# Kernel optimization log

Hardware: AMD Instinct MI355X
Metric: run time of the kernel (lower is better)

The kernel has to match this reference:

```python
import jax, jax.numpy as jnp
import numpy as np

B, N, D, H = 8, 2048, 256, 8
HD = D // H  # head_dim = 32
LN_EPS = 1e-5


def setup_inputs() -> dict:
    key = jax.random.key(0)
    ks = jax.random.split(key, 8)
    x = jax.random.normal(ks[0], (B, N, D), dtype=jnp.float32)
    # dense 0/1 adjacency with guaranteed self-loops (avoids all -inf softmax rows)
    adj = jax.random.randint(ks[1], (B, N, N), 0, 2, dtype=jnp.int32)
    adj = jnp.maximum(adj, jnp.eye(N, dtype=jnp.int32)[None, :, :])
    s = 0.02
    Wq = jax.random.normal(ks[2], (D, D), dtype=jnp.float32) * s
    Wk = jax.random.normal(ks[3], (D, D), dtype=jnp.float32) * s
    Wv = jax.random.normal(ks[4], (D, D), dtype=jnp.float32) * s
    Wo = jax.random.normal(ks[5], (D, D), dtype=jnp.float32) * s
    zeros = jnp.zeros((D,), dtype=jnp.float32)
    return {
        "x": x, "adjacency": adj,
        "Wq": Wq, "bq": zeros, "Wk": Wk, "bk": zeros,
        "Wv": Wv, "bv": zeros, "Wo": Wo, "bo": zeros,
        "gamma": jnp.ones((D,), dtype=jnp.float32), "beta": zeros,
    }


def reference(x, adjacency, Wq, bq, Wk, bk, Wv, bv, Wo, bo, gamma, beta):
    b, n, d = x.shape
    q = (x @ Wq + bq).reshape(b, n, H, HD)
    k = (x @ Wk + bk).reshape(b, n, H, HD)
    v = (x @ Wv + bv).reshape(b, n, H, HD)
    # scores: [B, N(query), M(key), H]
    scores = jnp.einsum('bnhd,bmhd->bnmh', q, k) / jnp.sqrt(jnp.float32(HD))
    mask = (adjacency == 0)[..., None]  # [B,N,M,1] broadcasts over heads
    scores = jnp.where(mask, -jnp.inf, scores)
    weights = jax.nn.softmax(scores, axis=2)  # softmax over key axis m
    # dropout is identity in eval mode
    attended = jnp.einsum('bnmh,bmhd->bnhd', weights, v).reshape(b, n, d)
    out = attended @ Wo + bo
    out = out + x  # residual (output.shape == x.shape since input_dim == output_dim)
    mu = jnp.mean(out, axis=-1, keepdims=True)
    var = jnp.mean(jnp.square(out - mu), axis=-1, keepdims=True)
    return (out - mu) * jax.lax.rsqrt(var + LN_EPS) * gamma + beta
```

## Files before the change

### kernel.cpp

```cpp
#include <hip/hip_runtime.h>
#include <hip/hip_bf16.h>
#include <cstdint>
#include <cstddef>

#define B_ 8
#define N_ 2048
#define D_ 256
#define H_ 8
#define HD_ 32
#define LN_EPS 1e-5f
#define QSCALE 0.25506275f

typedef __attribute__((ext_vector_type(8))) short short8;
typedef __attribute__((ext_vector_type(4))) float f32x4;
typedef __attribute__((ext_vector_type(16))) float f32x16;

static __device__ __forceinline__ float exp2v(float x) {
#if __has_builtin(__builtin_amdgcn_exp2f)
    return __builtin_amdgcn_exp2f(x);
#else
    float r;
    asm("v_exp_f32 %0, %1" : "=v"(r) : "v"(x));
    return r;
#endif
}

static __device__ __forceinline__ unsigned short f2bf(float f) {
    union { float f; unsigned int u; } v; v.f = f;
    unsigned int r = v.u + 0x7fffu + ((v.u >> 16) & 1u);
    return (unsigned short)(r >> 16);
}

static __device__ __forceinline__ unsigned int cvtpk(float lo, float hi) {
    unsigned int d;
    asm("v_cvt_pk_bf16_f32 %0, %1, %2" : "=v"(d) : "v"(lo), "v"(hi));
    return d;
}

__global__ __launch_bounds__(256) void k_prep_w(const float* __restrict__ w0, const float* __restrict__ w1,
                                                const float* __restrict__ w2, const float* __restrict__ w3,
                                                unsigned short* __restrict__ wt) {
    int c = blockIdx.x, mat = blockIdx.y, k = threadIdx.x;
    const float* w = (mat == 0) ? w0 : (mat == 1) ? w1 : (mat == 2) ? w2 : w3;
    wt[((size_t)(mat * 256 + c)) * 256 + k] = f2bf(w[k * 256 + c]);
}

__global__ __launch_bounds__(256) void k_maskF(const int* __restrict__ adj,
                                               unsigned int* __restrict__ mbgT2) {
    __shared__ unsigned int bits[64][66];
    int tid = threadIdx.x, lane = tid & 63, wv = tid >> 6;
    int b = blockIdx.x >> 5, rg = blockIdx.x & 31;

    const int* base = adj + ((size_t)(b * N_ + rg * 64 + wv * 16)) * N_ + lane;
#pragma unroll 1
    for (int i = 0; i < 16; ++i) {
        const int* prow = base + (size_t)i * N_;
#pragma unroll
        for (int half = 0; half < 2; ++half) {
            int v[16];
#pragma unroll
            for (int j = 0; j < 16; ++j)
                v[j] = prow[half * 1024 + j * 64];
            __builtin_amdgcn_sched_barrier(0);
#pragma unroll
            for (int j = 0; j < 16; ++j) {
                unsigned long long m = __ballot(v[j] != 0);
                if (lane == 0)
                    *reinterpret_cast<unsigned long long*>(&bits[wv * 16 + i][half * 32 + 2 * j]) = m;
            }
        }
    }
    __syncthreads();

    int h = lane >> 5, l31 = lane & 31;
    const unsigned int M[5] = {0x0000FFFFu, 0x00FF00FFu, 0x0F0F0F0Fu, 0x33333333u, 0x55555555u};
#pragma unroll
    for (int j = 0; j < 16; ++j) {
        int kw = wv * 16 + j;
        unsigned int w = bits[lane][kw];
#pragma unroll
        for (int si = 0; si < 5; ++si) {
            int s = 16 >> si;
            unsigned int m = M[si];
            unsigned int t = (unsigned int)__shfl_xor((int)w, s, 64);
            unsigned int a = (w & m) | ((t & m) << s);
            unsigned int c = (w & ~m) | ((t >> s) & m);
            w = (lane & s) ? c : a;
        }
        int k = kw * 32 + l31;
        int kp = (k & ~7) | ((k & 3) << 1) | ((k >> 2) & 1);
        mbgT2[((size_t)(b * 64 + rg * 2 + h)) * 2048 + kp] = w;
    }
}

__global__ __launch_bounds__(256) void k_qkv(const float* __restrict__ x,
                                             const unsigned short* __restrict__ wt,
                                             const float* __restrict__ bq, const float* __restrict__ bk,
                                             const float* __restrict__ bv,
                                             unsigned short* __restrict__ Qb, unsigned short* __restrict__ Kb,
                                             unsigned short* __restrict__ Vs) {
    int mat = blockIdx.y;
    int lane = threadIdx.x & 63;
    int wv = threadIdx.x >> 6;
    int row0 = blockIdx.x * 64 + wv * 16;
    int l15 = lane & 15, lg = lane >> 4;
    const float* bias = (mat == 0) ? bq : (mat == 1) ? bk : bv;
    const float qs = (mat == 0) ? QSCALE : 1.0f;
    const unsigned short* wm = wt + (size_t)mat * 65536;

    short8 af[8];
    const float* xrow = x + (size_t)(row0 + l15) * 256 + lg * 8;
#pragma unroll
    for (int kk = 0; kk < 8; ++kk) {
        float4 a = *reinterpret_cast<const float4*>(xrow + kk * 32);
        float4 b = *reinterpret_cast<const float4*>(xrow + kk * 32 + 4);
        union { short8 s8; unsigned int u[4]; } t;
        t.u[0] = cvtpk(a.x, a.y); t.u[1] = cvtpk(a.z, a.w);
        t.u[2] = cvtpk(b.x, b.y); t.u[3] = cvtpk(b.z, b.w);
        af[kk] = t.s8;
    }

    int b = row0 >> 11;
    int nbase = (row0 & 2047) + lg * 4;

    for (int ci = 0; ci < 16; ++ci) {
        const unsigned short* wrow = wm + (size_t)(ci * 16 + l15) * 256 + lg * 8;
        f32x4 acc = {0.f, 0.f, 0.f, 0.f};
#pragma unroll
        for (int kk = 0; kk < 8; ++kk) {
            short8 bfg = *reinterpret_cast<const short8*>(wrow + kk * 32);
            acc = __builtin_amdgcn_mfma_f32_16x16x32_bf16(af[kk], bfg, acc, 0, 0, 0);
        }
        int col = ci * 16 + l15;
        float bcol = bias[col];
        int h = col >> 5, hd = col & 31;
        if (mat < 2) {
            unsigned short* dst = (mat == 0) ? Qb : Kb;
#pragma unroll
            for (int r = 0; r < 4; ++r) {
                size_t off = ((size_t)(b * 8 + h) * 2048 + nbase + r) * 32 + hd;
                dst[off] = f2bf((acc[r] + bcol) * qs);
            }
        } else {
            size_t off = (size_t)(b * 8 + h) * 65536
                       + ((size_t)(nbase >> 4) * 32 + hd) * 16 + (nbase & 15);
            ushort4 o;
            o.x = f2bf(acc[0] + bcol); o.y = f2bf(acc[1] + bcol);
            o.z = f2bf(acc[2] + bcol); o.w = f2bf(acc[3] + bcol);
            *reinterpret_cast<ushort4*>(Vs + off) = o;
        }
    }
}

#define SL(j, offs) asm("s_load_dwordx2 %0, %1, " offs : "=s"(m##j) : "s"(mbase))
#define SLOAD16() do { \
    SL(0, "0x0");  SL(1, "0x8");  SL(2, "0x10"); SL(3, "0x18"); \
    SL(4, "0x20"); SL(5, "0x28"); SL(6, "0x30"); SL(7, "0x38"); \
    SL(8, "0x40"); SL(9, "0x48"); SL(10, "0x50"); SL(11, "0x58"); \
    SL(12, "0x60"); SL(13, "0x68"); SL(14, "0x70"); SL(15, "0x78"); } while (0)
#define CND(d, s_, mj) asm("v_cndmask_b32 %0, 0, %1, %2" : "=v"(d) : "v"(s_), "s"(mj))

__global__ __launch_bounds__(256, 5) void k_attn(const unsigned short* __restrict__ Qb,
                                                 const unsigned short* __restrict__ Kb,
                                                 const unsigned short* __restrict__ Vs,
                                                 const unsigned int* __restrict__ mbgT2,
                                                 unsigned short* __restrict__ att) {
    int tid = threadIdx.x;
    int lane = tid & 63;
    int l31 = lane & 31, hi = lane >> 5;
    int b = blockIdx.x & 7;
    int hg = (blockIdx.x >> 3) & 1;
    int qt32 = blockIdx.x >> 4;
    int q0 = qt32 * 32;
    int head = hg * 4 + (tid >> 6);
    int bh = b * 8 + head;

    const unsigned short* Qh = Qb + (size_t)bh * N_ * HD_;
    const unsigned short* Kh = Kb + (size_t)bh * N_ * HD_;
    const unsigned short* Vh = Vs + (size_t)bh * 65536;

    short8 qf0 = *reinterpret_cast<const short8*>(Qh + (size_t)(q0 + l31) * HD_ + hi * 8);
    short8 qf1 = *reinterpret_cast<const short8*>(Qh + (size_t)(q0 + l31) * HD_ + hi * 8 + 16);
    const unsigned short* krow = Kh + (size_t)l31 * HD_ + hi * 8;
    const unsigned short* vfp = Vh + (size_t)l31 * 16 + hi * 8;

    unsigned long long mbase = (unsigned long long)(mbgT2 + (size_t)(b * 64 + qt32) * 2048);
    unsigned long long m0, m1, m2, m3, m4, m5, m6, m7, m8, m9, m10, m11, m12, m13, m14, m15;
    SLOAD16();

    const f32x16 fz = {0.f,0.f,0.f,0.f,0.f,0.f,0.f,0.f,0.f,0.f,0.f,0.f,0.f,0.f,0.f,0.f};
    f32x16 attacc = fz;
    float lsum = 0.f;

#pragma unroll 2
    for (int t = 0; t < 64; ++t) {
        short8 kf0 = *reinterpret_cast<const short8*>(krow + (size_t)t * 1024);
        short8 kf1 = *reinterpret_cast<const short8*>(krow + (size_t)t * 1024 + 16);
        short8 vf0 = *reinterpret_cast<const short8*>(vfp + (size_t)t * 1024);
        short8 vf1 = *reinterpret_cast<const short8*>(vfp + (size_t)t * 1024 + 512);

        f32x16 s = __builtin_amdgcn_mfma_f32_32x32x16_bf16(kf0, qf0, fz, 0, 0, 0);
        s = __builtin_amdgcn_mfma_f32_32x32x16_bf16(kf1, qf1, s, 0, 0, 0);

        float e0 = exp2v(s[0]),  e1 = exp2v(s[1]),  e2 = exp2v(s[2]),  e3 = exp2v(s[3]);
        float e4 = exp2v(s[4]),  e5 = exp2v(s[5]),  e6 = exp2v(s[6]),  e7 = exp2v(s[7]);
        float e8 = exp2v(s[8]),  e9 = exp2v(s[9]),  e10 = exp2v(s[10]), e11 = exp2v(s[11]);
        float e12 = exp2v(s[12]), e13 = exp2v(s[13]), e14 = exp2v(s[14]), e15 = exp2v(s[15]);

        asm volatile("s_waitcnt lgkmcnt(0)"
                     : "+s"(m0), "+s"(m1), "+s"(m2), "+s"(m3), "+s"(m4), "+s"(m5), "+s"(m6), "+s"(m7),
                       "+s"(m8), "+s"(m9), "+s"(m10), "+s"(m11), "+s"(m12), "+s"(m13), "+s"(m14), "+s"(m15));

        float p0, p1, p2, p3, p4, p5, p6, p7, p8, p9, p10, p11, p12, p13, p14, p15;
        CND(p0, e0, m0);   CND(p1, e1, m1);   CND(p2, e2, m2);   CND(p3, e3, m3);
        CND(p4, e4, m4);   CND(p5, e5, m5);   CND(p6, e6, m6);   CND(p7, e7, m7);
        CND(p8, e8, m8);   CND(p9, e9, m9);   CND(p10, e10, m10); CND(p11, e11, m11);
        CND(p12, e12, m12); CND(p13, e13, m13); CND(p14, e14, m14); CND(p15, e15, m15);

        lsum += ((p0 + p1) + (p2 + p3)) + ((p4 + p5) + (p6 + p7))
              + ((p8 + p9) + (p10 + p11)) + ((p12 + p13) + (p14 + p15));

        unsigned int pd[4][2];
        pd[0][0] = cvtpk(p0, p1);   pd[0][1] = cvtpk(p2, p3);
        pd[1][0] = cvtpk(p4, p5);   pd[1][1] = cvtpk(p6, p7);
        pd[2][0] = cvtpk(p8, p9);   pd[2][1] = cvtpk(p10, p11);
        pd[3][0] = cvtpk(p12, p13); pd[3][1] = cvtpk(p14, p15);

        mbase += 128;
        SLOAD16();

        asm("v_permlane32_swap_b32 %0, %1" : "+v"(pd[0][0]), "+v"(pd[1][0]));
        asm("v_permlane32_swap_b32 %0, %1" : "+v"(pd[0][1]), "+v"(pd[1][1]));
        asm("v_permlane32_swap_b32 %0, %1" : "+v"(pd[2][0]), "+v"(pd[3][0]));
        asm("v_permlane32_swap_b32 %0, %1" : "+v"(pd[2][1]), "+v"(pd[3][1]));

        union { short8 s8; unsigned int u[4]; } bf0, bf1;
        bf0.u[0] = pd[0][0]; bf0.u[1] = pd[0][1]; bf0.u[2] = pd[1][0]; bf0.u[3] = pd[1][1];
        bf1.u[0] = pd[2][0]; bf1.u[1] = pd[2][1]; bf1.u[2] = pd[3][0]; bf1.u[3] = pd[3][1];

        attacc = __builtin_amdgcn_mfma_f32_32x32x16_bf16(vf0, bf0.s8, attacc, 0, 0, 0);
        attacc = __builtin_amdgcn_mfma_f32_32x32x16_bf16(vf1, bf1.s8, attacc, 0, 0, 0);
    }

    lsum += __shfl_xor(lsum, 32, 64);
    float rcp = 1.f / lsum;

    unsigned short* arow = att + ((size_t)b * N_ + q0 + l31) * D_ + head * HD_;
#pragma unroll
    for (int g = 0; g < 4; ++g) {
        ushort4 o;
        o.x = f2bf(attacc[4 * g + 0] * rcp);
        o.y = f2bf(attacc[4 * g + 1] * rcp);
        o.z = f2bf(attacc[4 * g + 2] * rcp);
        o.w = f2bf(attacc[4 * g + 3] * rcp);
        *reinterpret_cast<ushort4*>(arow + 8 * g + 4 * hi) = o;
    }
}

__global__ __launch_bounds__(256) void k_outln(const unsigned short* __restrict__ att,
                                               const unsigned short* __restrict__ wot,
                                               const float* __restrict__ bo,
                                               const float* __restrict__ x,
                                               const float* __restrict__ gamma, const float* __restrict__ beta,
                                               float* __restrict__ out) {
    int lane = threadIdx.x & 63, wv = threadIdx.x >> 6;
    int l15 = lane & 15, lg = lane >> 4;
    int row0 = blockIdx.x * 64 + wv * 16;

    short8 af[8];
    const unsigned short* arow = att + (size_t)(row0 + l15) * 256 + lg * 8;
#pragma unroll
    for (int kk = 0; kk < 8; ++kk)
        af[kk] = *reinterpret_cast<const short8*>(arow + kk * 32);

    float v[16][4];
#pragma unroll
    for (int ci = 0; ci < 16; ++ci) {
        const unsigned short* wrow = wot + (size_t)(ci * 16 + l15) * 256 + lg * 8;
        f32x4 acc = {0.f, 0.f, 0.f, 0.f};
#pragma unroll
        for (int kk = 0; kk < 8; ++kk) {
            short8 bfg = *reinterpret_cast<const short8*>(wrow + kk * 32);
            acc = __builtin_amdgcn_mfma_f32_16x16x32_bf16(af[kk], bfg, acc, 0, 0, 0);
        }
        float bcol = bo[ci * 16 + l15];
#pragma unroll
        for (int r = 0; r < 4; ++r)
            v[ci][r] = acc[r] + bcol + x[(size_t)(row0 + lg * 4 + r) * 256 + ci * 16 + l15];
    }

    float sum[4] = {0.f, 0.f, 0.f, 0.f}, sq[4] = {0.f, 0.f, 0.f, 0.f};
#pragma unroll
    for (int ci = 0; ci < 16; ++ci)
#pragma unroll
        for (int r = 0; r < 4; ++r) {
            sum[r] += v[ci][r];
            sq[r] += v[ci][r] * v[ci][r];
        }
#pragma unroll
    for (int d = 1; d < 16; d <<= 1)
#pragma unroll
        for (int r = 0; r < 4; ++r) {
            sum[r] += __shfl_xor(sum[r], d, 64);
            sq[r] += __shfl_xor(sq[r], d, 64);
        }

    float mu[4], rs[4];
#pragma unroll
    for (int r = 0; r < 4; ++r) {
        mu[r] = sum[r] * (1.f / 256.f);
        float var = sq[r] * (1.f / 256.f) - mu[r] * mu[r];
        rs[r] = rsqrtf(var + LN_EPS);
    }

#pragma unroll
    for (int ci = 0; ci < 16; ++ci) {
        float g = gamma[ci * 16 + l15], be = beta[ci * 16 + l15];
#pragma unroll
        for (int r = 0; r < 4; ++r)
            out[(size_t)(row0 + lg * 4 + r) * 256 + ci * 16 + l15] = (v[ci][r] - mu[r]) * rs[r] * g + be;
    }
}

extern "C" void kernel_launch(void* const* d_in, const int* in_sizes, int n_in,
                              void* d_out, int out_size, void* d_ws, size_t ws_size,
                              hipStream_t stream) {
    (void)in_sizes; (void)n_in; (void)out_size; (void)ws_size;
    const float* x     = (const float*)d_in[0];
    const int*   adj   = (const int*)d_in[1];
    const float* Wq    = (const float*)d_in[2];
    const float* bq    = (const float*)d_in[3];
    const float* Wk    = (const float*)d_in[4];
    const float* bk    = (const float*)d_in[5];
    const float* Wv    = (const float*)d_in[6];
    const float* bv    = (const float*)d_in[7];
    const float* Wo    = (const float*)d_in[8];
    const float* bo    = (const float*)d_in[9];
    const float* gamma = (const float*)d_in[10];
    const float* beta  = (const float*)d_in[11];
    float* out = (float*)d_out;

    char* ws = (char*)d_ws;
    unsigned short* wt   = (unsigned short*)ws; ws += (size_t)4 * 256 * 256 * 2;
    unsigned short* Qb   = (unsigned short*)ws; ws += (size_t)B_ * H_ * N_ * HD_ * 2;
    unsigned short* Kb   = (unsigned short*)ws; ws += (size_t)B_ * H_ * N_ * HD_ * 2;
    unsigned short* Vs   = (unsigned short*)ws; ws += (size_t)B_ * H_ * N_ * HD_ * 2;
    unsigned short* att  = (unsigned short*)ws; ws += (size_t)16384 * 256 * 2;
    unsigned int*   mbgT2 = (unsigned int*)ws;  ws += (size_t)B_ * 64 * 2048 * 4 + 8192;

    k_prep_w<<<dim3(256, 4), 256, 0, stream>>>(Wq, Wk, Wv, Wo, wt);
    k_maskF<<<256, 256, 0, stream>>>(adj, mbgT2);
    k_qkv<<<dim3(256, 3), 256, 0, stream>>>(x, wt, bq, bk, bv, Qb, Kb, Vs);
    k_attn<<<1024, 256, 0, stream>>>(Qb, Kb, Vs, mbgT2, att);
    k_outln<<<256, 256, 0, stream>>>(att, wt + 3 * 65536, bo, x, gamma, beta, out);
}
```

Baseline: 187.8 us.

## Store Q/K/V in fragment-swizzled layout, vectorize stores, widen mask kernel

Q and K are now written by k_qkv in the same 32-row tiled, fragment-ordered layout as V, using swapped MFMA operands so each lane emits a contiguous ushort4 store. This lets k_attn fetch Q/K fragments with lane-linear contiguous loads instead of strided row loads. The output LayerNorm kernel also swaps MFMA operands so each lane owns one row, giving float4 loads and stores of x, gamma, beta and out and a shorter cross-lane reduction. The mask kernel doubles its threads per block to 512, so each wave handles half as many rows. The layout change must stay consistent across producer and consumer or attention results will be wrong.

```diff
diff --git a/kernel.cpp b/kernel.cpp
--- a/kernel.cpp
+++ b/kernel.cpp
@@ -45,15 +45,15 @@
     wt[((size_t)(mat * 256 + c)) * 256 + k] = f2bf(w[k * 256 + c]);
 }
 
-__global__ __launch_bounds__(256) void k_maskF(const int* __restrict__ adj,
+__global__ __launch_bounds__(512) void k_maskF(const int* __restrict__ adj,
                                                unsigned int* __restrict__ mbgT2) {
     __shared__ unsigned int bits[64][66];
     int tid = threadIdx.x, lane = tid & 63, wv = tid >> 6;
     int b = blockIdx.x >> 5, rg = blockIdx.x & 31;
 
-    const int* base = adj + ((size_t)(b * N_ + rg * 64 + wv * 16)) * N_ + lane;
+    const int* base = adj + ((size_t)(b * N_ + rg * 64 + wv * 8)) * N_ + lane;
 #pragma unroll 1
-    for (int i = 0; i < 16; ++i) {
+    for (int i = 0; i < 8; ++i) {
         const int* prow = base + (size_t)i * N_;
 #pragma unroll
         for (int half = 0; half < 2; ++half) {
@@ -66,7 +66,7 @@
             for (int j = 0; j < 16; ++j) {
                 unsigned long long m = __ballot(v[j] != 0);
                 if (lane == 0)
-                    *reinterpret_cast<unsigned long long*>(&bits[wv * 16 + i][half * 32 + 2 * j]) = m;
+                    *reinterpret_cast<unsigned long long*>(&bits[wv * 8 + i][half * 32 + 2 * j]) = m;
             }
         }
     }
@@ -75,8 +75,8 @@
     int h = lane >> 5, l31 = lane & 31;
     const unsigned int M[5] = {0x0000FFFFu, 0x00FF00FFu, 0x0F0F0F0Fu, 0x33333333u, 0x55555555u};
 #pragma unroll
-    for (int j = 0; j < 16; ++j) {
-        int kw = wv * 16 + j;
+    for (int j = 0; j < 8; ++j) {
+        int kw = wv * 8 + j;
         unsigned int w = bits[lane][kw];
 #pragma unroll
         for (int si = 0; si < 5; ++si) {
@@ -97,7 +97,7 @@
                                              const unsigned short* __restrict__ wt,
                                              const float* __restrict__ bq, const float* __restrict__ bk,
                                              const float* __restrict__ bv,
-                                             unsigned short* __restrict__ Qb, unsigned short* __restrict__ Kb,
+                                             unsigned short* __restrict__ Qts, unsigned short* __restrict__ Ks,
                                              unsigned short* __restrict__ Vs) {
     int mat = blockIdx.y;
     int lane = threadIdx.x & 63;
@@ -123,27 +123,44 @@
     int b = row0 >> 11;
     int nbase = (row0 & 2047) + lg * 4;
 
-    for (int ci = 0; ci < 16; ++ci) {
-        const unsigned short* wrow = wm + (size_t)(ci * 16 + l15) * 256 + lg * 8;
-        f32x4 acc = {0.f, 0.f, 0.f, 0.f};
-#pragma unroll
-        for (int kk = 0; kk < 8; ++kk) {
-            short8 bfg = *reinterpret_cast<const short8*>(wrow + kk * 32);
-            acc = __builtin_amdgcn_mfma_f32_16x16x32_bf16(af[kk], bfg, acc, 0, 0, 0);
-        }
-        int col = ci * 16 + l15;
-        float bcol = bias[col];
-        int h = col >> 5, hd = col & 31;
-        if (mat < 2) {
-            unsigned short* dst = (mat == 0) ? Qb : Kb;
-#pragma unroll
-            for (int r = 0; r < 4; ++r) {
-                size_t off = ((size_t)(b * 8 + h) * 2048 + nbase + r) * 32 + hd;
-                dst[off] = f2bf((acc[r] + bcol) * qs);
+    if (mat < 2) {
+        unsigned short* dst = (mat == 0) ? Qts : Ks;
+        int n = (row0 & 2047) + l15;
+        for (int ci = 0; ci < 16; ++ci) {
+            const unsigned short* wrow = wm + (size_t)(ci * 16 + l15) * 256 + lg * 8;
+            f32x4 acc = {0.f, 0.f, 0.f, 0.f};
+#pragma unroll
+            for (int kk = 0; kk < 8; ++kk) {
+                short8 bfg = *reinterpret_cast<const short8*>(wrow + kk * 32);
+                acc = __builtin_amdgcn_mfma_f32_16x16x32_bf16(bfg, af[kk], acc, 0, 0, 0);
             }
-        } else {
-            size_t off = (size_t)(b * 8 + h) * 65536
-                       + ((size_t)(nbase >> 4) * 32 + hd) * 16 + (nbase & 15);
+            int col0 = ci * 16 + lg * 4;
+            float4 b4 = *reinterpret_cast<const float4*>(bias + col0);
+            int h = col0 >> 5;
+            int hd0 = col0 & 31;
+            size_t off = (size_t)(b * 8 + h) * 65536 + (size_t)(n >> 5) * 1024
+                       + (size_t)(hd0 >> 4) * 512
+                       + (size_t)((((hd0 >> 3) & 1) * 32 + (n & 31))) * 8 + (hd0 & 7);
+            ushort4 o;
+            o.x = f2bf((acc[0] + b4.x) * qs); o.y = f2bf((acc[1] + b4.y) * qs);
+            o.z = f2bf((acc[2] + b4.z) * qs); o.w = f2bf((acc[3] + b4.w) * qs);
+            *reinterpret_cast<ushort4*>(dst + off) = o;
+        }
+    } else {
+        for (int ci = 0; ci < 16; ++ci) {
+            const unsigned short* wrow = wm + (size_t)(ci * 16 + l15) * 256 + lg * 8;
+            f32x4 acc = {0.f, 0.f, 0.f, 0.f};
+#pragma unroll
+            for (int kk = 0; kk < 8; ++kk) {
+                short8 bfg = *reinterpret_cast<const short8*>(wrow + kk * 32);
+                acc = __builtin_amdgcn_mfma_f32_16x16x32_bf16(af[kk], bfg, acc, 0, 0, 0);
+            }
+            int col = ci * 16 + l15;
+            float bcol = bias[col];
+            int h = col >> 5, hd = col & 31;
+            int posb = nbase & 31;
+            size_t off = (size_t)(b * 8 + h) * 65536 + (size_t)(nbase >> 5) * 1024
+                       + (posb >> 4) * 512 + ((((posb >> 3) & 1) * 32 + hd)) * 8 + (posb & 7);
             ushort4 o;
             o.x = f2bf(acc[0] + bcol); o.y = f2bf(acc[1] + bcol);
             o.z = f2bf(acc[2] + bcol); o.w = f2bf(acc[3] + bcol);
@@ -160,7 +177,7 @@
     SL(12, "0x60"); SL(13, "0x68"); SL(14, "0x70"); SL(15, "0x78"); } while (0)
 #define CND(d, s_, mj) asm("v_cndmask_b32 %0, 0, %1, %2" : "=v"(d) : "v"(s_), "s"(mj))
 
-__global__ __launch_bounds__(256, 5) void k_attn(const unsigned short* __restrict__ Qb,
+__global__ __launch_bounds__(256, 5) void k_attn(const unsigned short* __restrict__ Qts,
                                                  const unsigned short* __restrict__ Kb,
                                                  const unsigned short* __restrict__ Vs,
                                                  const unsigned int* __restrict__ mbgT2,
@@ -175,14 +192,14 @@
     int head = hg * 4 + (tid >> 6);
     int bh = b * 8 + head;
 
-    const unsigned short* Qh = Qb + (size_t)bh * N_ * HD_;
-    const unsigned short* Kh = Kb + (size_t)bh * N_ * HD_;
+    const unsigned short* Qh = Qts + (size_t)bh * 65536 + (size_t)qt32 * 1024 + (size_t)lane * 8;
+    const unsigned short* Kh = Kb + (size_t)bh * 65536;
     const unsigned short* Vh = Vs + (size_t)bh * 65536;
 
-    short8 qf0 = *reinterpret_cast<const short8*>(Qh + (size_t)(q0 + l31) * HD_ + hi * 8);
-    short8 qf1 = *reinterpret_cast<const short8*>(Qh + (size_t)(q0 + l31) * HD_ + hi * 8 + 16);
-    const unsigned short* krow = Kh + (size_t)l31 * HD_ + hi * 8;
-    const unsigned short* vfp = Vh + (size_t)l31 * 16 + hi * 8;
+    short8 qf0 = *reinterpret_cast<const short8*>(Qh);
+    short8 qf1 = *reinterpret_cast<const short8*>(Qh + 512);
+    const unsigned short* krow = Kh + (size_t)lane * 8;
+    const unsigned short* vfp = Vh + (size_t)lane * 8;
 
     unsigned long long mbase = (unsigned long long)(mbgT2 + (size_t)(b * 64 + qt32) * 2048);
     unsigned long long m0, m1, m2, m3, m4, m5, m6, m7, m8, m9, m10, m11, m12, m13, m14, m15;
@@ -195,7 +212,7 @@
 #pragma unroll 2
     for (int t = 0; t < 64; ++t) {
         short8 kf0 = *reinterpret_cast<const short8*>(krow + (size_t)t * 1024);
-        short8 kf1 = *reinterpret_cast<const short8*>(krow + (size_t)t * 1024 + 16);
+        short8 kf1 = *reinterpret_cast<const short8*>(krow + (size_t)t * 1024 + 512);
         short8 vf0 = *reinterpret_cast<const short8*>(vfp + (size_t)t * 1024);
         short8 vf1 = *reinterpret_cast<const short8*>(vfp + (size_t)t * 1024 + 512);
 
@@ -266,14 +283,16 @@
     int lane = threadIdx.x & 63, wv = threadIdx.x >> 6;
     int l15 = lane & 15, lg = lane >> 4;
     int row0 = blockIdx.x * 64 + wv * 16;
+    size_t row = (size_t)(row0 + l15);
 
     short8 af[8];
-    const unsigned short* arow = att + (size_t)(row0 + l15) * 256 + lg * 8;
+    const unsigned short* arow = att + row * 256 + lg * 8;
 #pragma unroll
     for (int kk = 0; kk < 8; ++kk)
         af[kk] = *reinterpret_cast<const short8*>(arow + kk * 32);
 
     float v[16][4];
+    float sum = 0.f, sq = 0.f;
 #pragma unroll
     for (int ci = 0; ci < 16; ++ci) {
         const unsigned short* wrow = wot + (size_t)(ci * 16 + l15) * 256 + lg * 8;
@@ -281,44 +300,40 @@
 #pragma unroll
         for (int kk = 0; kk < 8; ++kk) {
             short8 bfg = *reinterpret_cast<const short8*>(wrow + kk * 32);
-            acc = __builtin_amdgcn_mfma_f32_16x16x32_bf16(af[kk], bfg, acc, 0, 0, 0);
-        }
-        float bcol = bo[ci * 16 + l15];
-#pragma unroll
-        for (int r = 0; r < 4; ++r)
-            v[ci][r] = acc[r] + bcol + x[(size_t)(row0 + lg * 4 + r) * 256 + ci * 16 + l15];
-    }
-
-    float sum[4] = {0.f, 0.f, 0.f, 0.f}, sq[4] = {0.f, 0.f, 0.f, 0.f};
-#pragma unroll
-    for (int ci = 0; ci < 16; ++ci)
+            acc = __builtin_amdgcn_mfma_f32_16x16x32_bf16(bfg, af[kk], acc, 0, 0, 0);
+        }
+        int col0 = ci * 16 + lg * 4;
+        float4 b4 = *reinterpret_cast<const float4*>(bo + col0);
+        float4 x4 = *reinterpret_cast<const float4*>(x + row * 256 + col0);
+        v[ci][0] = acc[0] + b4.x + x4.x;
+        v[ci][1] = acc[1] + b4.y + x4.y;
+        v[ci][2] = acc[2] + b4.z + x4.z;
+        v[ci][3] = acc[3] + b4.w + x4.w;
 #pragma unroll
         for (int r = 0; r < 4; ++r) {
-            sum[r] += v[ci][r];
-            sq[r] += v[ci][r] * v[ci][r];
-        }
-#pragma unroll
-    for (int d = 1; d < 16; d <<= 1)
-#pragma unroll
-        for (int r = 0; r < 4; ++r) {
-            sum[r] += __shfl_xor(sum[r], d, 64);
-            sq[r] += __shfl_xor(sq[r], d, 64);
-        }
-
-    float mu[4], rs[4];
-#pragma unroll
-    for (int r = 0; r < 4; ++r) {
-        mu[r] = sum[r] * (1.f / 256.f);
-        float var = sq[r] * (1.f / 256.f) - mu[r] * mu[r];
-        rs[r] = rsqrtf(var + LN_EPS);
-    }
+            sum += v[ci][r];
+            sq += v[ci][r] * v[ci][r];
+        }
+    }
+
+    sum += __shfl_xor(sum, 16, 64); sq += __shfl_xor(sq, 16, 64);
+    sum += __shfl_xor(sum, 32, 64); sq += __shfl_xor(sq, 32, 64);
+
+    float mu = sum * (1.f / 256.f);
+    float var = sq * (1.f / 256.f) - mu * mu;
+    float rs = rsqrtf(var + LN_EPS);
 
 #pragma unroll
     for (int ci = 0; ci < 16; ++ci) {
-        float g = gamma[ci * 16 + l15], be = beta[ci * 16 + l15];
-#pragma unroll
-        for (int r = 0; r < 4; ++r)
-            out[(size_t)(row0 + lg * 4 + r) * 256 + ci * 16 + l15] = (v[ci][r] - mu[r]) * rs[r] * g + be;
+        int col0 = ci * 16 + lg * 4;
+        float4 g4 = *reinterpret_cast<const float4*>(gamma + col0);
+        float4 be4 = *reinterpret_cast<const float4*>(beta + col0);
+        float4 o;
+        o.x = (v[ci][0] - mu) * rs * g4.x + be4.x;
+        o.y = (v[ci][1] - mu) * rs * g4.y + be4.y;
+        o.z = (v[ci][2] - mu) * rs * g4.z + be4.z;
+        o.w = (v[ci][3] - mu) * rs * g4.w + be4.w;
+        *reinterpret_cast<float4*>(out + row * 256 + col0) = o;
     }
 }
 
@@ -342,15 +357,15 @@
 
     char* ws = (char*)d_ws;
     unsigned short* wt   = (unsigned short*)ws; ws += (size_t)4 * 256 * 256 * 2;
-    unsigned short* Qb   = (unsigned short*)ws; ws += (size_t)B_ * H_ * N_ * HD_ * 2;
-    unsigned short* Kb   = (unsigned short*)ws; ws += (size_t)B_ * H_ * N_ * HD_ * 2;
+    unsigned short* Qts  = (unsigned short*)ws; ws += (size_t)B_ * H_ * N_ * HD_ * 2;
+    unsigned short* Ks   = (unsigned short*)ws; ws += (size_t)B_ * H_ * N_ * HD_ * 2;
     unsigned short* Vs   = (unsigned short*)ws; ws += (size_t)B_ * H_ * N_ * HD_ * 2;
     unsigned short* att  = (unsigned short*)ws; ws += (size_t)16384 * 256 * 2;
     unsigned int*   mbgT2 = (unsigned int*)ws;  ws += (size_t)B_ * 64 * 2048 * 4 + 8192;
 
     k_prep_w<<<dim3(256, 4), 256, 0, stream>>>(Wq, Wk, Wv, Wo, wt);
-    k_maskF<<<256, 256, 0, stream>>>(adj, mbgT2);
-    k_qkv<<<dim3(256, 3), 256, 0, stream>>>(x, wt, bq, bk, bv, Qb, Kb, Vs);
-    k_attn<<<1024, 256, 0, stream>>>(Qb, Kb, Vs, mbgT2, att);
+    k_maskF<<<256, 512, 0, stream>>>(adj, mbgT2);
+    k_qkv<<<dim3(256, 3), 256, 0, stream>>>(x, wt, bq, bk, bv, Qts, Ks, Vs);
+    k_attn<<<1024, 256, 0, stream>>>(Qts, Ks, Vs, mbgT2, att);
     k_outln<<<256, 256, 0, stream>>>(att, wt + 3 * 65536, bo, x, gamma, beta, out);
 }
```

After: 176.0 us, median of 3. 1.07x faster.
